# Kernel optimization log

Hardware: AMD Instinct MI355X
Metric: run time of the kernel (lower is better)

Reference implementation:

```python
import jax, jax.numpy as jnp
import numpy as np

POS_DIM, COND_DIM, VIEW_DIM, HID = 3, 64, 3, 128
N_DENSITY, N_COLOR, SKIP = 8, 3, 4
DIN = POS_DIM + COND_DIM            # 67, density input dim
CIN = HID + VIEW_DIM                # 131, color input dim


def setup_inputs() -> dict:
    key = jax.random.key(0)
    ks = iter(jax.random.split(key, 64))

    def w(shape):
        return jax.random.normal(next(ks), shape, dtype=jnp.float32) * 0.05

    inp = {
        "pos": jax.random.normal(next(ks), (2048, 128, POS_DIM), dtype=jnp.float32),
        "cond": jax.random.normal(next(ks), (COND_DIM,), dtype=jnp.float32),
        "view": jax.random.normal(next(ks), (2048, VIEW_DIM), dtype=jnp.float32),
    }
    # density trunk: layer 0 takes DIN; layer SKIP+1 takes HID+DIN (skip concat); rest HID
    d_ins = [DIN] + [HID + DIN if i == SKIP + 1 else HID for i in range(1, N_DENSITY)]
    for i, din in enumerate(d_ins):
        inp[f"dW{i}"] = w((din, HID))
        inp[f"db{i}"] = w((HID,))
    inp["sW"], inp["sb"] = w((HID, 1)), w((1,))
    # color trunk
    c_ins = [CIN] + [HID // 2] * (N_COLOR - 1)
    for i, cin in enumerate(c_ins):
        inp[f"cW{i}"] = w((cin, HID // 2))
        inp[f"cb{i}"] = w((HID // 2,))
    inp["rW"], inp["rb"] = w((HID // 2, 3)), w((3,))
    return inp


def reference(pos, cond, view,
              dW0, db0, dW1, db1, dW2, db2, dW3, db3,
              dW4, db4, dW5, db5, dW6, db6, dW7, db7,
              sW, sb, cW0, cb0, cW1, cb1, cW2, cb2, rW, rb):
    bs, n_sample, _ = pos.shape
    cond_e = jnp.broadcast_to(cond[None, None, :], (bs, n_sample, COND_DIM))
    view_e = jnp.broadcast_to(view[:, None, :], (bs, n_sample, VIEW_DIM))

    x0 = jnp.concatenate([pos, cond_e], axis=-1)  # [bs, n, DIN]
    dWs = [dW0, dW1, dW2, dW3, dW4, dW5, dW6, dW7]
    dbs = [db0, db1, db2, db3, db4, db5, db6, db7]

    h = x0
    for i in range(N_DENSITY):
        h = jax.nn.relu(h @ dWs[i] + dbs[i])
        if i == SKIP:
            h = jnp.concatenate([x0, h], axis=-1)  # skip concat, input first
    sigma = h @ sW + sb  # [bs, n, 1]

    h = jnp.concatenate([h, view_e], axis=-1)  # [bs, n, CIN]
    cWs, cbs = [cW0, cW1, cW2], [cb0, cb1, cb2]
    for i in range(N_COLOR):
        h = jax.nn.relu(h @ cWs[i] + cbs[i])
    rgb = h @ rW + rb  # [bs, n, 3]

    return jnp.concatenate([rgb, sigma], axis=-1)  # [bs, n, 4]
```

## Files before the change

kernel.cpp:

```cpp
#include <hip/hip_runtime.h>

typedef _Float16 f16;
typedef _Float16 f16x8 __attribute__((ext_vector_type(8)));
typedef __fp16 hf16x2 __attribute__((ext_vector_type(2)));
typedef float f32x4 __attribute__((ext_vector_type(4)));
typedef float f32x16 __attribute__((ext_vector_type(16)));

#define WS_PARAMS 262144

struct Ptrs { const float* p[29]; };

__device__ __forceinline__ int klog32(int q) {
  return (q & ~12) | ((q & 4) << 1) | ((q & 8) >> 1);
}

__global__ void nerf_prep(Ptrs ptrs, char* __restrict__ ws) {
  const int t = threadIdx.x;
  if (blockIdx.x == 0) {
    float* P = (float*)(ws + WS_PARAMS);
    const float* cond = ptrs.p[1];
    const float* dW0 = ptrs.p[3];  const float* db0 = ptrs.p[4];
    const float* dW5 = ptrs.p[13]; const float* db5 = ptrs.p[14];
    if (t < 128) {
      float a0 = db0[t], a5 = db5[t];
      for (int k = 0; k < 64; ++k) {
        const float c = cond[k];
        a0 += c * dW0[(3 + k) * 128 + t];
        a5 += c * dW5[(3 + k) * 128 + t];
      }
      P[t] = a0;
      P[512 + t] = a5;
      for (int k = 0; k < 3; ++k) {
        P[128 + k * 128 + t] = dW0[k * 128 + t];
        P[640 + k * 128 + t] = dW5[k * 128 + t];
      }
      P[1024 + t] = ptrs.p[6][t];
      P[1152 + t] = ptrs.p[8][t];
      P[1280 + t] = ptrs.p[10][t];
      P[1408 + t] = ptrs.p[12][t];
      P[1536 + t] = ptrs.p[16][t];
      P[1664 + t] = ptrs.p[18][t];
      P[2176 + t] = ptrs.p[19][t];
    }
    if (t < 64) {
      P[1792 + t] = ptrs.p[22][t];
      for (int k = 0; k < 3; ++k)
        P[1856 + k * 64 + t] = ptrs.p[21][(128 + k) * 64 + t];
      P[2048 + t] = ptrs.p[24][t];
      P[2112 + t] = ptrs.p[26][t];
      for (int c = 0; c < 3; ++c)
        P[2308 + c * 64 + t] = ptrs.p[27][t * 3 + c];
    }
    if (t == 0) {
      P[2304] = ptrs.p[20][0];
      P[2500] = ptrs.p[28][0];
      P[2501] = ptrs.p[28][1];
      P[2502] = ptrs.p[28][2];
    }
    if (t < 3)  P[2305 + t] = 0.f;
    if (t < 57) P[2503 + t] = 0.f;
    return;
  }
  const int e = (blockIdx.x - 1) * 256 + t;
  float v; int dst;
  if (e < 114688) {
    const int img = e >> 14, o = e & 16383;
    const int j = o & 7, lane = (o >> 3) & 63, m = (o >> 9) & 7, T = o >> 12;
    const int kraw = m * 16 + ((lane >> 5) << 3) + j;
    const int k = (img == 0) ? kraw : klog32(kraw);
    const int och = T * 32 + (lane & 31);
    v = ptrs.p[5 + 2 * img][(k + (img == 4 ? 67 : 0)) * 128 + och];
    dst = img * 32768 + (((T * 8 + m) * 64 + lane) << 4) + (j << 1);
  } else if (e < 122880) {
    const int o = e - 114688;
    const int j = o & 7, lane = (o >> 3) & 63, m = (o >> 9) & 7, T = o >> 12;
    const int k = klog32(m * 16 + ((lane >> 5) << 3) + j);
    const int och = T * 32 + (lane & 31);
    v = ptrs.p[21][k * 64 + och];
    dst = 229376 + (((T * 8 + m) * 64 + lane) << 4) + (j << 1);
  } else if (e < 126976) {
    const int o = e - 122880;
    const int j = o & 7, lane = (o >> 3) & 63, m = (o >> 9) & 3, T = o >> 11;
    const int k = klog32(m * 16 + ((lane >> 5) << 3) + j);
    const int och = T * 32 + (lane & 31);
    v = ptrs.p[23][k * 64 + och];
    dst = 245760 + (((T * 4 + m) * 64 + lane) << 4) + (j << 1);
  } else {
    const int o = e - 126976;
    const int j = o & 7, lane = (o >> 3) & 63, m = (o >> 9) & 3, T = o >> 11;
    const int k = klog32(m * 16 + ((lane >> 5) << 3) + j);
    const int och = T * 32 + (lane & 31);
    v = ptrs.p[25][k * 64 + och];
    dst = 253952 + (((T * 4 + m) * 64 + lane) << 4) + (j << 1);
  }
  *(f16*)(ws + dst) = (f16)v;
}

__device__ __forceinline__ void loadF4(f16x8* A, const char* __restrict__ img,
                                       int fb, int lane) {
#pragma unroll
  for (int i = 0; i < 4; ++i)
    A[i] = *(const f16x8*)(img + (((fb + i) * 64 + lane) << 4));
}

__device__ __forceinline__ f16x8 packRelu(const f32x4 v0, const f32x4 v1) {
  const hf16x2 p0 = __builtin_amdgcn_cvt_pkrtz(v0[0], v0[1]);
  const hf16x2 p1 = __builtin_amdgcn_cvt_pkrtz(v0[2], v0[3]);
  const hf16x2 p2 = __builtin_amdgcn_cvt_pkrtz(v1[0], v1[1]);
  const hf16x2 p3 = __builtin_amdgcn_cvt_pkrtz(v1[2], v1[3]);
  f16x8 hb;
  hb[0] = (f16)p0[0]; hb[1] = (f16)p0[1]; hb[2] = (f16)p1[0]; hb[3] = (f16)p1[1];
  hb[4] = (f16)p2[0]; hb[5] = (f16)p2[1]; hb[6] = (f16)p3[0]; hb[7] = (f16)p3[1];
#pragma unroll
  for (int e2 = 0; e2 < 8; ++e2)
    hb[e2] = hb[e2] > (f16)0.f ? hb[e2] : (f16)0.f;
  return hb;
}

template<int T, int KH, int INIT>
__device__ __forceinline__ void qL32(const f16x8 B[2][8], f32x16 acc[2][4],
                                     const f16x8* A, const float* __restrict__ P,
                                     const float px[2][3],
                                     const float* __restrict__ vw2,
                                     int biasOff, int h4, int wbase) {
  if (KH == 0) {
    f32x4 bq[4];
#pragma unroll
    for (int q = 0; q < 4; ++q)
      bq[q] = *(const f32x4*)(P + biasOff + T * 32 + q * 8 + h4);
    f32x4 e0[4], e1[4], e2[4];
    if (INIT == 1) {
#pragma unroll
      for (int q = 0; q < 4; ++q) {
        e0[q] = *(const f32x4*)(P + 640 + T * 32 + q * 8 + h4);
        e1[q] = *(const f32x4*)(P + 768 + T * 32 + q * 8 + h4);
        e2[q] = *(const f32x4*)(P + 896 + T * 32 + q * 8 + h4);
      }
    } else if (INIT == 2) {
#pragma unroll
      for (int q = 0; q < 4; ++q) {
        e0[q] = *(const f32x4*)(P + 1856 + T * 32 + q * 8 + h4);
        e1[q] = *(const f32x4*)(P + 1920 + T * 32 + q * 8 + h4);
        e2[q] = *(const f32x4*)(P + 1984 + T * 32 + q * 8 + h4);
      }
    }
    __builtin_amdgcn_s_setprio(1);
#pragma unroll
    for (int pt = 0; pt < 2; ++pt) {
      f32x16 s;
#pragma unroll
      for (int q = 0; q < 4; ++q) {
        f32x4 vq = bq[q];
        if (INIT == 1)
          vq += px[pt][0] * e0[q] + px[pt][1] * e1[q] + px[pt][2] * e2[q];
        if (INIT == 2) {
          const int ray = (wbase + pt * 32) >> 7;
          vq += vw2[ray * 3] * e0[q] + vw2[ray * 3 + 1] * e1[q]
              + vw2[ray * 3 + 2] * e2[q];
        }
#pragma unroll
        for (int e3 = 0; e3 < 4; ++e3) s[q * 4 + e3] = vq[e3];
      }
      acc[pt][T] = __builtin_amdgcn_mfma_f32_32x32x16_f16(A[0], B[pt][KH * 4 + 0],
                                                          s, 0, 0, 0);
    }
#pragma unroll
    for (int i = 1; i < 4; ++i)
#pragma unroll
      for (int pt = 0; pt < 2; ++pt)
        acc[pt][T] = __builtin_amdgcn_mfma_f32_32x32x16_f16(
            A[i], B[pt][KH * 4 + i], acc[pt][T], 0, 0, 0);
    __builtin_amdgcn_s_setprio(0);
  } else {
    __builtin_amdgcn_s_setprio(1);
#pragma unroll
    for (int i = 0; i < 4; ++i)
#pragma unroll
      for (int pt = 0; pt < 2; ++pt)
        acc[pt][T] = __builtin_amdgcn_mfma_f32_32x32x16_f16(
            A[i], B[pt][KH * 4 + i], acc[pt][T], 0, 0, 0);
    __builtin_amdgcn_s_setprio(0);
  }
}

template<int T>
__device__ __forceinline__ void toBtile(const f32x16 acc[2][4], f16x8 B[2][8]) {
#pragma unroll
  for (int pt = 0; pt < 2; ++pt) {
    f32x4 v0, v1, v2, v3;
#pragma unroll
    for (int e3 = 0; e3 < 4; ++e3) {
      v0[e3] = acc[pt][T][e3];
      v1[e3] = acc[pt][T][4 + e3];
      v2[e3] = acc[pt][T][8 + e3];
      v3[e3] = acc[pt][T][12 + e3];
    }
    B[pt][2 * T]     = packRelu(v0, v1);
    B[pt][2 * T + 1] = packRelu(v2, v3);
  }
}

template<int NM>
__device__ __forceinline__ void toB32(const f32x16 acc[2][4], f16x8 B[2][8]) {
#pragma unroll
  for (int pt = 0; pt < 2; ++pt)
#pragma unroll
    for (int m = 0; m < NM; ++m) {
      const int s = (m & 1) * 8;
      f32x4 v0, v1;
#pragma unroll
      for (int e3 = 0; e3 < 4; ++e3) {
        v0[e3] = acc[pt][m >> 1][s + e3];
        v1[e3] = acc[pt][m >> 1][s + 4 + e3];
      }
      B[pt][m] = packRelu(v0, v1);
    }
}

__global__ __launch_bounds__(512, 2) void nerf_main(
    const float* __restrict__ pos, const float* __restrict__ view,
    const char* __restrict__ ws, float* __restrict__ out) {
  __shared__ __align__(16) float Lp[2560 + 1536 + 16];
  const int t = threadIdx.x, lane = t & 63, w = t >> 6;
  const int c32 = lane & 31;
  const int h4 = ((lane >> 5) << 2), h8 = ((lane >> 5) << 3);
  const int base = blockIdx.x * 512;
  const int wbase = w * 64;
  const float* P = Lp;
  float* Lpos = Lp + 2560;
  float* Lvw = Lp + 4096;

  for (int i = t; i < 2560; i += 512) Lp[i] = ((const float*)(ws + WS_PARAMS))[i];
  for (int i = t; i < 1536; i += 512) Lpos[i] = pos[base * 3 + i];
  if (t < 12) Lvw[t] = view[(base >> 7) * 3 + t];
  __syncthreads();

  f16x8 Aa[4], Ab[4];
  loadF4(Aa, ws + 0, 0, lane);

  float px[2][3];
#pragma unroll
  for (int pt = 0; pt < 2; ++pt) {
    const int lp = wbase + pt * 32 + c32;
#pragma unroll
    for (int d = 0; d < 3; ++d) px[pt][d] = Lpos[lp * 3 + d];
  }

  f16x8 Bx[2][8], By[2][8];
#pragma unroll
  for (int m = 0; m < 8; ++m) {
    const int chb = m * 16 + h8;
    const f32x4 b0  = *(const f32x4*)(P + chb),       b1  = *(const f32x4*)(P + chb + 4);
    const f32x4 w00 = *(const f32x4*)(P + 128 + chb), w01 = *(const f32x4*)(P + 128 + chb + 4);
    const f32x4 w10 = *(const f32x4*)(P + 256 + chb), w11 = *(const f32x4*)(P + 256 + chb + 4);
    const f32x4 w20 = *(const f32x4*)(P + 384 + chb), w21 = *(const f32x4*)(P + 384 + chb + 4);
#pragma unroll
    for (int pt = 0; pt < 2; ++pt) {
      const f32x4 v0 = b0 + px[pt][0] * w00 + px[pt][1] * w10 + px[pt][2] * w20;
      const f32x4 v1 = b1 + px[pt][0] * w01 + px[pt][1] * w11 + px[pt][2] * w21;
      Bx[pt][m] = packRelu(v0, v1);
    }
  }

  f32x16 acc[2][4];

#define DLAYER(Bin, Bout, img_, imgNext, BIAS, INIT_)                          \
  loadF4(Ab, img_,  4, lane); qL32<0,0,INIT_>(Bin, acc, Aa, P, px, Lvw, BIAS, h4, wbase); \
  loadF4(Aa, img_,  8, lane); qL32<0,1,INIT_>(Bin, acc, Ab, P, px, Lvw, BIAS, h4, wbase); \
  toBtile<0>(acc, Bout);                                                       \
  loadF4(Ab, img_, 12, lane); qL32<1,0,INIT_>(Bin, acc, Aa, P, px, Lvw, BIAS, h4, wbase); \
  loadF4(Aa, img_, 16, lane); qL32<1,1,INIT_>(Bin, acc, Ab, P, px, Lvw, BIAS, h4, wbase); \
  toBtile<1>(acc, Bout);                                                       \
  loadF4(Ab, img_, 20, lane); qL32<2,0,INIT_>(Bin, acc, Aa, P, px, Lvw, BIAS, h4, wbase); \
  loadF4(Aa, img_, 24, lane); qL32<2,1,INIT_>(Bin, acc, Ab, P, px, Lvw, BIAS, h4, wbase); \
  toBtile<2>(acc, Bout);                                                       \
  loadF4(Ab, img_, 28, lane); qL32<3,0,INIT_>(Bin, acc, Aa, P, px, Lvw, BIAS, h4, wbase); \
  loadF4(Aa, imgNext, 0, lane); qL32<3,1,INIT_>(Bin, acc, Ab, P, px, Lvw, BIAS, h4, wbase); \
  toBtile<3>(acc, Bout);

#define DLAYER_NOOUT(Bin, img_, imgNext, BIAS, INIT_)                          \
  loadF4(Ab, img_,  4, lane); qL32<0,0,INIT_>(Bin, acc, Aa, P, px, Lvw, BIAS, h4, wbase); \
  loadF4(Aa, img_,  8, lane); qL32<0,1,INIT_>(Bin, acc, Ab, P, px, Lvw, BIAS, h4, wbase); \
  loadF4(Ab, img_, 12, lane); qL32<1,0,INIT_>(Bin, acc, Aa, P, px, Lvw, BIAS, h4, wbase); \
  loadF4(Aa, img_, 16, lane); qL32<1,1,INIT_>(Bin, acc, Ab, P, px, Lvw, BIAS, h4, wbase); \
  loadF4(Ab, img_, 20, lane); qL32<2,0,INIT_>(Bin, acc, Aa, P, px, Lvw, BIAS, h4, wbase); \
  loadF4(Aa, img_, 24, lane); qL32<2,1,INIT_>(Bin, acc, Ab, P, px, Lvw, BIAS, h4, wbase); \
  loadF4(Ab, img_, 28, lane); qL32<3,0,INIT_>(Bin, acc, Aa, P, px, Lvw, BIAS, h4, wbase); \
  loadF4(Aa, imgNext, 0, lane); qL32<3,1,INIT_>(Bin, acc, Ab, P, px, Lvw, BIAS, h4, wbase);

  DLAYER(Bx, By, ws +      0, ws +  32768, 1024, 0)
  DLAYER(By, Bx, ws +  32768, ws +  65536, 1152, 0)
  DLAYER(Bx, By, ws +  65536, ws +  98304, 1280, 0)
  DLAYER(By, Bx, ws +  98304, ws + 131072, 1408, 0)
  DLAYER(Bx, By, ws + 131072, ws + 163840,  512, 1)
  DLAYER(By, Bx, ws + 163840, ws + 196608, 1536, 0)
  DLAYER_NOOUT(Bx, ws + 196608, ws + 229376, 1664, 0)
#undef DLAYER
#undef DLAYER_NOOUT

  float sig[2];
#pragma unroll
  for (int pt = 0; pt < 2; ++pt) {
    float s = 0.f;
#pragma unroll
    for (int T = 0; T < 4; ++T)
#pragma unroll
      for (int q = 0; q < 4; ++q) {
        const f32x4 wq = *(const f32x4*)(P + 2176 + T * 32 + q * 8 + h4);
#pragma unroll
        for (int e3 = 0; e3 < 4; ++e3)
          s += fmaxf(acc[pt][T][q * 4 + e3], 0.f) * wq[e3];
      }
    s += __shfl_xor(s, 32);
    sig[pt] = s + P[2304];
  }
  toB32<8>(acc, By);

  loadF4(Ab, ws + 229376,  4, lane);
  qL32<0, 0, 2>(By, acc, Aa, P, px, Lvw, 1792, h4, wbase);
  loadF4(Aa, ws + 229376,  8, lane);
  qL32<0, 1, 2>(By, acc, Ab, P, px, Lvw, 1792, h4, wbase);
  toBtile<0>(acc, Bx);
  loadF4(Ab, ws + 229376, 12, lane);
  qL32<1, 0, 2>(By, acc, Aa, P, px, Lvw, 1792, h4, wbase);
  loadF4(Aa, ws + 245760,  0, lane);
  qL32<1, 1, 2>(By, acc, Ab, P, px, Lvw, 1792, h4, wbase);
  toBtile<1>(acc, Bx);

  loadF4(Ab, ws + 245760, 4, lane);
  qL32<0, 0, 0>(Bx, acc, Aa, P, px, Lvw, 2048, h4, wbase);
  toBtile<0>(acc, By);
  loadF4(Aa, ws + 253952, 0, lane);
  qL32<1, 0, 0>(Bx, acc, Ab, P, px, Lvw, 2048, h4, wbase);
  toBtile<1>(acc, By);

  loadF4(Ab, ws + 253952, 4, lane);
  qL32<0, 0, 0>(By, acc, Aa, P, px, Lvw, 2112, h4, wbase);
  qL32<1, 0, 0>(By, acc, Ab, P, px, Lvw, 2112, h4, wbase);

#pragma unroll
  for (int pt = 0; pt < 2; ++pt) {
    float a0 = 0.f, a1 = 0.f, a2 = 0.f;
#pragma unroll
    for (int T = 0; T < 2; ++T)
#pragma unroll
      for (int q = 0; q < 4; ++q) {
        const int ob = T * 32 + q * 8 + h4;
        const f32x4 r0 = *(const f32x4*)(P + 2308 + ob);
        const f32x4 r1 = *(const f32x4*)(P + 2372 + ob);
        const f32x4 r2 = *(const f32x4*)(P + 2436 + ob);
#pragma unroll
        for (int e3 = 0; e3 < 4; ++e3) {
          const float h = fmaxf(acc[pt][T][q * 4 + e3], 0.f);
          a0 += h * r0[e3]; a1 += h * r1[e3]; a2 += h * r2[e3];
        }
      }
    a0 += __shfl_xor(a0, 32);
    a1 += __shfl_xor(a1, 32);
    a2 += __shfl_xor(a2, 32);
    if (lane < 32) {
      float4 o;
      o.x = a0 + P[2500]; o.y = a1 + P[2501]; o.z = a2 + P[2502]; o.w = sig[pt];
      *(float4*)(out + (base + wbase + pt * 32 + c32) * 4) = o;
    }
  }
}

extern "C" void kernel_launch(void* const* d_in, const int* in_sizes, int n_in,
                              void* d_out, int out_size, void* d_ws, size_t ws_size,
                              hipStream_t stream) {
  Ptrs ptrs;
  for (int i = 0; i < 29; ++i) ptrs.p[i] = (const float*)d_in[i];
  char* ws = (char*)d_ws;
  nerf_prep<<<513, 256, 0, stream>>>(ptrs, ws);
  nerf_main<<<512, 512, 0, stream>>>((const float*)d_in[0], (const float*)d_in[2],
                                     ws, (float*)d_out);
}
```

Measured before the change: 80.93 us.

## Shrink accumulators to one tile and deepen weight-fragment prefetch to four buffers

Replaces the four-tile accumulator array with a single 32-column accumulator per point-tile that is converted to the next layer's B fragments right after each output tile finishes. The sigma and RGB heads are folded into per-tile partial dot products so the full hidden state is never held in registers. The register space this frees funds four rotating A-fragment buffers loaded two chunks ahead, instead of two buffers one chunk ahead, to hide global weight-load latency. The trade is more live prefetch registers and a tighter chain between each MFMA tile and the conversion that reads it.

```diff
diff --git a/kernel.cpp b/kernel.cpp
--- a/kernel.cpp
+++ b/kernel.cpp
@@ -117,31 +117,31 @@
   return hb;
 }
 
-template<int T, int KH, int INIT>
-__device__ __forceinline__ void qL32(const f16x8 B[2][8], f32x16 acc[2][4],
-                                     const f16x8* A, const float* __restrict__ P,
-                                     const float px[2][3],
-                                     const float* __restrict__ vw2,
-                                     int biasOff, int h4, int wbase) {
+template<int KH, int INIT>
+__device__ __forceinline__ void qL32s(const f16x8 B[2][8], f32x16 acc1[2],
+                                      const f16x8* A, const float* __restrict__ P,
+                                      const float px[2][3],
+                                      const float* __restrict__ vw2,
+                                      int biasOff, int ob, int h4, int wbase) {
   if (KH == 0) {
     f32x4 bq[4];
 #pragma unroll
     for (int q = 0; q < 4; ++q)
-      bq[q] = *(const f32x4*)(P + biasOff + T * 32 + q * 8 + h4);
+      bq[q] = *(const f32x4*)(P + biasOff + ob + q * 8 + h4);
     f32x4 e0[4], e1[4], e2[4];
     if (INIT == 1) {
 #pragma unroll
       for (int q = 0; q < 4; ++q) {
-        e0[q] = *(const f32x4*)(P + 640 + T * 32 + q * 8 + h4);
-        e1[q] = *(const f32x4*)(P + 768 + T * 32 + q * 8 + h4);
-        e2[q] = *(const f32x4*)(P + 896 + T * 32 + q * 8 + h4);
+        e0[q] = *(const f32x4*)(P + 640 + ob + q * 8 + h4);
+        e1[q] = *(const f32x4*)(P + 768 + ob + q * 8 + h4);
+        e2[q] = *(const f32x4*)(P + 896 + ob + q * 8 + h4);
       }
     } else if (INIT == 2) {
 #pragma unroll
       for (int q = 0; q < 4; ++q) {
-        e0[q] = *(const f32x4*)(P + 1856 + T * 32 + q * 8 + h4);
-        e1[q] = *(const f32x4*)(P + 1920 + T * 32 + q * 8 + h4);
-        e2[q] = *(const f32x4*)(P + 1984 + T * 32 + q * 8 + h4);
+        e0[q] = *(const f32x4*)(P + 1856 + ob + q * 8 + h4);
+        e1[q] = *(const f32x4*)(P + 1920 + ob + q * 8 + h4);
+        e2[q] = *(const f32x4*)(P + 1984 + ob + q * 8 + h4);
       }
     }
     __builtin_amdgcn_s_setprio(1);
@@ -161,15 +161,15 @@
 #pragma unroll
         for (int e3 = 0; e3 < 4; ++e3) s[q * 4 + e3] = vq[e3];
       }
-      acc[pt][T] = __builtin_amdgcn_mfma_f32_32x32x16_f16(A[0], B[pt][KH * 4 + 0],
-                                                          s, 0, 0, 0);
+      acc1[pt] = __builtin_amdgcn_mfma_f32_32x32x16_f16(A[0], B[pt][KH * 4 + 0],
+                                                        s, 0, 0, 0);
     }
 #pragma unroll
     for (int i = 1; i < 4; ++i)
 #pragma unroll
       for (int pt = 0; pt < 2; ++pt)
-        acc[pt][T] = __builtin_amdgcn_mfma_f32_32x32x16_f16(
-            A[i], B[pt][KH * 4 + i], acc[pt][T], 0, 0, 0);
+        acc1[pt] = __builtin_amdgcn_mfma_f32_32x32x16_f16(
+            A[i], B[pt][KH * 4 + i], acc1[pt], 0, 0, 0);
     __builtin_amdgcn_s_setprio(0);
   } else {
     __builtin_amdgcn_s_setprio(1);
@@ -177,44 +177,67 @@
     for (int i = 0; i < 4; ++i)
 #pragma unroll
       for (int pt = 0; pt < 2; ++pt)
-        acc[pt][T] = __builtin_amdgcn_mfma_f32_32x32x16_f16(
-            A[i], B[pt][KH * 4 + i], acc[pt][T], 0, 0, 0);
+        acc1[pt] = __builtin_amdgcn_mfma_f32_32x32x16_f16(
+            A[i], B[pt][KH * 4 + i], acc1[pt], 0, 0, 0);
     __builtin_amdgcn_s_setprio(0);
   }
 }
 
 template<int T>
-__device__ __forceinline__ void toBtile(const f32x16 acc[2][4], f16x8 B[2][8]) {
+__device__ __forceinline__ void toBtileS(const f32x16 acc1[2], f16x8 B[2][8]) {
 #pragma unroll
   for (int pt = 0; pt < 2; ++pt) {
     f32x4 v0, v1, v2, v3;
 #pragma unroll
     for (int e3 = 0; e3 < 4; ++e3) {
-      v0[e3] = acc[pt][T][e3];
-      v1[e3] = acc[pt][T][4 + e3];
-      v2[e3] = acc[pt][T][8 + e3];
-      v3[e3] = acc[pt][T][12 + e3];
+      v0[e3] = acc1[pt][e3];
+      v1[e3] = acc1[pt][4 + e3];
+      v2[e3] = acc1[pt][8 + e3];
+      v3[e3] = acc1[pt][12 + e3];
     }
     B[pt][2 * T]     = packRelu(v0, v1);
     B[pt][2 * T + 1] = packRelu(v2, v3);
   }
 }
 
-template<int NM>
-__device__ __forceinline__ void toB32(const f32x16 acc[2][4], f16x8 B[2][8]) {
-#pragma unroll
-  for (int pt = 0; pt < 2; ++pt)
-#pragma unroll
-    for (int m = 0; m < NM; ++m) {
-      const int s = (m & 1) * 8;
-      f32x4 v0, v1;
+template<int T>
+__device__ __forceinline__ void sigTile(const f32x16 acc1[2], float sig[2],
+                                        const float* __restrict__ P, int h4) {
+#pragma unroll
+  for (int pt = 0; pt < 2; ++pt) {
+    float s = sig[pt];
+#pragma unroll
+    for (int q = 0; q < 4; ++q) {
+      const f32x4 wq = *(const f32x4*)(P + 2176 + T * 32 + q * 8 + h4);
+#pragma unroll
+      for (int e3 = 0; e3 < 4; ++e3)
+        s += fmaxf(acc1[pt][q * 4 + e3], 0.f) * wq[e3];
+    }
+    sig[pt] = s;
+  }
+}
+
+template<int T>
+__device__ __forceinline__ void rgbTile(const f32x16 acc1[2], float r0[2],
+                                        float r1[2], float r2[2],
+                                        const float* __restrict__ P, int h4) {
+#pragma unroll
+  for (int pt = 0; pt < 2; ++pt) {
+    float a0 = r0[pt], a1 = r1[pt], a2 = r2[pt];
+#pragma unroll
+    for (int q = 0; q < 4; ++q) {
+      const int ob = T * 32 + q * 8 + h4;
+      const f32x4 w0 = *(const f32x4*)(P + 2308 + ob);
+      const f32x4 w1 = *(const f32x4*)(P + 2372 + ob);
+      const f32x4 w2 = *(const f32x4*)(P + 2436 + ob);
 #pragma unroll
       for (int e3 = 0; e3 < 4; ++e3) {
-        v0[e3] = acc[pt][m >> 1][s + e3];
-        v1[e3] = acc[pt][m >> 1][s + 4 + e3];
-      }
-      B[pt][m] = packRelu(v0, v1);
-    }
+        const float h = fmaxf(acc1[pt][q * 4 + e3], 0.f);
+        a0 += h * w0[e3]; a1 += h * w1[e3]; a2 += h * w2[e3];
+      }
+    }
+    r0[pt] = a0; r1[pt] = a1; r2[pt] = a2;
+  }
 }
 
 __global__ __launch_bounds__(512, 2) void nerf_main(
@@ -235,8 +258,11 @@
   if (t < 12) Lvw[t] = view[(base >> 7) * 3 + t];
   __syncthreads();
 
-  f16x8 Aa[4], Ab[4];
-  loadF4(Aa, ws + 0, 0, lane);
+  f16x8 Aa0[4], Aa1[4], Aa2[4], Aa3[4];
+  loadF4(Aa0, ws + 0, 0, lane);
+  loadF4(Aa1, ws + 0, 4, lane);
+  loadF4(Aa2, ws + 0, 8, lane);
+  loadF4(Aa3, ws + 0, 12, lane);
 
   float px[2][3];
 #pragma unroll
@@ -262,31 +288,43 @@
     }
   }
 
-  f32x16 acc[2][4];
+  f32x16 acc1[2];
+  float sig[2] = {0.f, 0.f};
+  float r0[2] = {0.f, 0.f}, r1[2] = {0.f, 0.f}, r2[2] = {0.f, 0.f};
+
+#define DCH(Ab_, imgN, fbN, Bin, KH_, INIT_, ob_, bias_)                       \
+  qL32s<KH_, INIT_>(Bin, acc1, Ab_, P, px, Lvw, bias_, ob_, h4, wbase);        \
+  loadF4(Ab_, imgN, fbN, lane);
+#define DCHN(Ab_, Bin, KH_, INIT_, ob_, bias_)                                 \
+  qL32s<KH_, INIT_>(Bin, acc1, Ab_, P, px, Lvw, bias_, ob_, h4, wbase);
 
 #define DLAYER(Bin, Bout, img_, imgNext, BIAS, INIT_)                          \
-  loadF4(Ab, img_,  4, lane); qL32<0,0,INIT_>(Bin, acc, Aa, P, px, Lvw, BIAS, h4, wbase); \
-  loadF4(Aa, img_,  8, lane); qL32<0,1,INIT_>(Bin, acc, Ab, P, px, Lvw, BIAS, h4, wbase); \
-  toBtile<0>(acc, Bout);                                                       \
-  loadF4(Ab, img_, 12, lane); qL32<1,0,INIT_>(Bin, acc, Aa, P, px, Lvw, BIAS, h4, wbase); \
-  loadF4(Aa, img_, 16, lane); qL32<1,1,INIT_>(Bin, acc, Ab, P, px, Lvw, BIAS, h4, wbase); \
-  toBtile<1>(acc, Bout);                                                       \
-  loadF4(Ab, img_, 20, lane); qL32<2,0,INIT_>(Bin, acc, Aa, P, px, Lvw, BIAS, h4, wbase); \
-  loadF4(Aa, img_, 24, lane); qL32<2,1,INIT_>(Bin, acc, Ab, P, px, Lvw, BIAS, h4, wbase); \
-  toBtile<2>(acc, Bout);                                                       \
-  loadF4(Ab, img_, 28, lane); qL32<3,0,INIT_>(Bin, acc, Aa, P, px, Lvw, BIAS, h4, wbase); \
-  loadF4(Aa, imgNext, 0, lane); qL32<3,1,INIT_>(Bin, acc, Ab, P, px, Lvw, BIAS, h4, wbase); \
-  toBtile<3>(acc, Bout);
-
-#define DLAYER_NOOUT(Bin, img_, imgNext, BIAS, INIT_)                          \
-  loadF4(Ab, img_,  4, lane); qL32<0,0,INIT_>(Bin, acc, Aa, P, px, Lvw, BIAS, h4, wbase); \
-  loadF4(Aa, img_,  8, lane); qL32<0,1,INIT_>(Bin, acc, Ab, P, px, Lvw, BIAS, h4, wbase); \
-  loadF4(Ab, img_, 12, lane); qL32<1,0,INIT_>(Bin, acc, Aa, P, px, Lvw, BIAS, h4, wbase); \
-  loadF4(Aa, img_, 16, lane); qL32<1,1,INIT_>(Bin, acc, Ab, P, px, Lvw, BIAS, h4, wbase); \
-  loadF4(Ab, img_, 20, lane); qL32<2,0,INIT_>(Bin, acc, Aa, P, px, Lvw, BIAS, h4, wbase); \
-  loadF4(Aa, img_, 24, lane); qL32<2,1,INIT_>(Bin, acc, Ab, P, px, Lvw, BIAS, h4, wbase); \
-  loadF4(Ab, img_, 28, lane); qL32<3,0,INIT_>(Bin, acc, Aa, P, px, Lvw, BIAS, h4, wbase); \
-  loadF4(Aa, imgNext, 0, lane); qL32<3,1,INIT_>(Bin, acc, Ab, P, px, Lvw, BIAS, h4, wbase);
+  DCH(Aa0, img_, 16, Bin, 0, INIT_,  0, BIAS)                                  \
+  DCH(Aa1, img_, 20, Bin, 1, INIT_,  0, BIAS)                                  \
+  toBtileS<0>(acc1, Bout);                                                     \
+  DCH(Aa2, img_, 24, Bin, 0, INIT_, 32, BIAS)                                  \
+  DCH(Aa3, img_, 28, Bin, 1, INIT_, 32, BIAS)                                  \
+  toBtileS<1>(acc1, Bout);                                                     \
+  DCH(Aa0, imgNext, 0, Bin, 0, INIT_, 64, BIAS)                                \
+  DCH(Aa1, imgNext, 4, Bin, 1, INIT_, 64, BIAS)                                \
+  toBtileS<2>(acc1, Bout);                                                     \
+  DCH(Aa2, imgNext, 8, Bin, 0, INIT_, 96, BIAS)                                \
+  DCH(Aa3, imgNext, 12, Bin, 1, INIT_, 96, BIAS)                               \
+  toBtileS<3>(acc1, Bout);
+
+#define DLAYER7(Bin, Bout, img_, imgNext, BIAS)                                \
+  DCH(Aa0, img_, 16, Bin, 0, 0,  0, BIAS)                                      \
+  DCH(Aa1, img_, 20, Bin, 1, 0,  0, BIAS)                                      \
+  sigTile<0>(acc1, sig, P, h4); toBtileS<0>(acc1, Bout);                       \
+  DCH(Aa2, img_, 24, Bin, 0, 0, 32, BIAS)                                      \
+  DCH(Aa3, img_, 28, Bin, 1, 0, 32, BIAS)                                      \
+  sigTile<1>(acc1, sig, P, h4); toBtileS<1>(acc1, Bout);                       \
+  DCH(Aa0, imgNext, 0, Bin, 0, 0, 64, BIAS)                                    \
+  DCH(Aa1, imgNext, 4, Bin, 1, 0, 64, BIAS)                                    \
+  sigTile<2>(acc1, sig, P, h4); toBtileS<2>(acc1, Bout);                       \
+  DCH(Aa2, imgNext, 8, Bin, 0, 0, 96, BIAS)                                    \
+  DCH(Aa3, imgNext, 12, Bin, 1, 0, 96, BIAS)                                   \
+  sigTile<3>(acc1, sig, P, h4); toBtileS<3>(acc1, Bout);
 
   DLAYER(Bx, By, ws +      0, ws +  32768, 1024, 0)
   DLAYER(By, Bx, ws +  32768, ws +  65536, 1152, 0)
@@ -294,67 +332,40 @@
   DLAYER(By, Bx, ws +  98304, ws + 131072, 1408, 0)
   DLAYER(Bx, By, ws + 131072, ws + 163840,  512, 1)
   DLAYER(By, Bx, ws + 163840, ws + 196608, 1536, 0)
-  DLAYER_NOOUT(Bx, ws + 196608, ws + 229376, 1664, 0)
-#undef DLAYER
-#undef DLAYER_NOOUT
-
-  float sig[2];
-#pragma unroll
-  for (int pt = 0; pt < 2; ++pt) {
-    float s = 0.f;
-#pragma unroll
-    for (int T = 0; T < 4; ++T)
-#pragma unroll
-      for (int q = 0; q < 4; ++q) {
-        const f32x4 wq = *(const f32x4*)(P + 2176 + T * 32 + q * 8 + h4);
-#pragma unroll
-        for (int e3 = 0; e3 < 4; ++e3)
-          s += fmaxf(acc[pt][T][q * 4 + e3], 0.f) * wq[e3];
-      }
+  DLAYER7(Bx, By, ws + 196608, ws + 229376, 1664)
+
+#pragma unroll
+  for (int pt = 0; pt < 2; ++pt) {
+    float s = sig[pt];
     s += __shfl_xor(s, 32);
     sig[pt] = s + P[2304];
   }
-  toB32<8>(acc, By);
-
-  loadF4(Ab, ws + 229376,  4, lane);
-  qL32<0, 0, 2>(By, acc, Aa, P, px, Lvw, 1792, h4, wbase);
-  loadF4(Aa, ws + 229376,  8, lane);
-  qL32<0, 1, 2>(By, acc, Ab, P, px, Lvw, 1792, h4, wbase);
-  toBtile<0>(acc, Bx);
-  loadF4(Ab, ws + 229376, 12, lane);
-  qL32<1, 0, 2>(By, acc, Aa, P, px, Lvw, 1792, h4, wbase);
-  loadF4(Aa, ws + 245760,  0, lane);
-  qL32<1, 1, 2>(By, acc, Ab, P, px, Lvw, 1792, h4, wbase);
-  toBtile<1>(acc, Bx);
-
-  loadF4(Ab, ws + 245760, 4, lane);
-  qL32<0, 0, 0>(Bx, acc, Aa, P, px, Lvw, 2048, h4, wbase);
-  toBtile<0>(acc, By);
-  loadF4(Aa, ws + 253952, 0, lane);
-  qL32<1, 0, 0>(Bx, acc, Ab, P, px, Lvw, 2048, h4, wbase);
-  toBtile<1>(acc, By);
-
-  loadF4(Ab, ws + 253952, 4, lane);
-  qL32<0, 0, 0>(By, acc, Aa, P, px, Lvw, 2112, h4, wbase);
-  qL32<1, 0, 0>(By, acc, Ab, P, px, Lvw, 2112, h4, wbase);
-
-#pragma unroll
-  for (int pt = 0; pt < 2; ++pt) {
-    float a0 = 0.f, a1 = 0.f, a2 = 0.f;
-#pragma unroll
-    for (int T = 0; T < 2; ++T)
-#pragma unroll
-      for (int q = 0; q < 4; ++q) {
-        const int ob = T * 32 + q * 8 + h4;
-        const f32x4 r0 = *(const f32x4*)(P + 2308 + ob);
-        const f32x4 r1 = *(const f32x4*)(P + 2372 + ob);
-        const f32x4 r2 = *(const f32x4*)(P + 2436 + ob);
-#pragma unroll
-        for (int e3 = 0; e3 < 4; ++e3) {
-          const float h = fmaxf(acc[pt][T][q * 4 + e3], 0.f);
-          a0 += h * r0[e3]; a1 += h * r1[e3]; a2 += h * r2[e3];
-        }
-      }
+
+  DCH(Aa0, ws + 245760, 0, By, 0, 2,  0, 1792)
+  DCH(Aa1, ws + 245760, 4, By, 1, 2,  0, 1792)
+  toBtileS<0>(acc1, Bx);
+  DCH(Aa2, ws + 253952, 0, By, 0, 2, 32, 1792)
+  DCH(Aa3, ws + 253952, 4, By, 1, 2, 32, 1792)
+  toBtileS<1>(acc1, Bx);
+
+  DCHN(Aa0, Bx, 0, 0,  0, 2048)
+  toBtileS<0>(acc1, By);
+  DCHN(Aa1, Bx, 0, 0, 32, 2048)
+  toBtileS<1>(acc1, By);
+
+  DCHN(Aa2, By, 0, 0,  0, 2112)
+  rgbTile<0>(acc1, r0, r1, r2, P, h4);
+  DCHN(Aa3, By, 0, 0, 32, 2112)
+  rgbTile<1>(acc1, r0, r1, r2, P, h4);
+
+#undef DCH
+#undef DCHN
+#undef DLAYER
+#undef DLAYER7
+
+#pragma unroll
+  for (int pt = 0; pt < 2; ++pt) {
+    float a0 = r0[pt], a1 = r1[pt], a2 = r2[pt];
     a0 += __shfl_xor(a0, 32);
     a1 += __shfl_xor(a1, 32);
     a2 += __shfl_xor(a2, 32);
```

Measured after the change: 118.3 us. 1.46x slower.
